# Performance work log

Hardware: AMD Instinct MI355X
Metric: run time of the kernel (lower is better)

## Reference

```python
import jax, jax.numpy as jnp
import numpy as np
import math

V = 32000      # vocab_size
CTX = 1025     # context_length (S = CTX-1)
L = 4          # num_layers
D = 1024       # hidden_dim
H = 16         # heads
DH = D // H    # head_dim
FF = 4 * D
B = 2
PAD = 3        # padding_idx / tokenizer.pad_id()


def setup_inputs() -> dict:
    key = jax.random.key(0)
    ks = jax.random.split(key, 16)
    g = lambda k, shape: jax.random.normal(k, shape, dtype=jnp.float32) * 0.02
    text = jax.random.randint(ks[0], (B, CTX), 0, V)
    emb = g(ks[1], (V, D)).at[PAD].set(0.0)   # nn.Embedding with padding_idx=3
    u = g(ks[2], (H, DH))
    v = g(ks[3], (H, DH))
    Wq = g(ks[4], (L, D, D))
    Wk = g(ks[5], (L, D, D))
    Wv = g(ks[6], (L, D, D))
    Wr = g(ks[7], (L, D, D))
    Wfc = g(ks[8], (L, D, D))
    bfc = jnp.zeros((L, D), jnp.float32)
    ln1g = jnp.ones((L, D), jnp.float32); ln1b = jnp.zeros((L, D), jnp.float32)
    ln2g = jnp.ones((L, D), jnp.float32); ln2b = jnp.zeros((L, D), jnp.float32)
    W1 = g(ks[9], (L, D, FF)); b1 = jnp.zeros((L, FF), jnp.float32)
    W2 = g(ks[10], (L, FF, D)); b2 = jnp.zeros((L, D), jnp.float32)
    lnfg = jnp.ones((D,), jnp.float32); lnfb = jnp.zeros((D,), jnp.float32)
    Wlm = g(ks[11], (D, V)); blm = jnp.zeros((V,), jnp.float32)
    return dict(text=text, emb=emb, u=u, v=v, Wq=Wq, Wk=Wk, Wv=Wv, Wr=Wr,
                Wfc=Wfc, bfc=bfc, ln1g=ln1g, ln1b=ln1b, ln2g=ln2g, ln2b=ln2b,
                W1=W1, b1=b1, W2=W2, b2=b2, lnfg=lnfg, lnfb=lnfb, Wlm=Wlm, blm=blm)


def _ln(x, g, b, eps=1e-5):
    m = x.mean(-1, keepdims=True)
    va = ((x - m) ** 2).mean(-1, keepdims=True)
    return (x - m) / jnp.sqrt(va + eps) * g + b


def _rel_shift(x):
    # Transformer-XL relative shift: pad a zero column, reshape, drop first row.
    b, h, s, r = x.shape
    xp = jnp.pad(x, ((0, 0), (0, 0), (0, 0), (1, 0)))     # (b,h,s,r+1)
    xp = xp.reshape(b, h, r + 1, s)
    return xp[:, :, 1:, :].reshape(b, h, s, r)


def _forward(text, emb, u, v, Wq, Wk, Wv, Wr, Wfc, bfc, ln1g, ln1b, ln2g, ln2b,
             W1, b1, W2, b2, lnfg, lnfb, Wlm, blm):
    ip = text[:, :-1]                 # ip_text = text[:, :-1]
    S = ip.shape[1]
    x = emb[ip]                       # (B,S,D)
    # PositionalEmbedding over Transformer-XL positions [S-1 .. 0]
    pos = jnp.arange(S - 1, -1, -1, dtype=jnp.float32)
    inv_freq = 1.0 / (10000.0 ** (jnp.arange(0, D, 2, dtype=jnp.float32) / D))
    sinu = pos[:, None] * inv_freq[None, :]
    rel = jnp.concatenate([jnp.sin(sinu), jnp.cos(sinu)], axis=-1)  # (S,D)
    # get_mask: causal triu OR pad-token rows
    causal = jnp.triu(jnp.ones((S, S), dtype=bool), 1)
    pad = (ip == PAD)
    mask = (pad[:, :, None] | causal[None]) [:, None, :, :]        # (B,1,S,S)
    full_row = mask.all(-1, keepdims=True)                          # fully-masked rows -> NaN-fill 0
    scale = 1.0 / math.sqrt(DH)
    for l in range(L):
        xn = _ln(x, ln1g[l], ln1b[l])
        q = (xn @ Wq[l]).reshape(B, S, H, DH).transpose(0, 2, 1, 3)   # (B,H,S,DH)
        k = (xn @ Wk[l]).reshape(B, S, H, DH).transpose(0, 2, 1, 3)
        vv = (xn @ Wv[l]).reshape(B, S, H, DH).transpose(0, 2, 1, 3)
        r = (rel @ Wr[l]).reshape(S, H, DH).transpose(1, 0, 2)        # (H,S,DH)
        term_AC = jnp.einsum('bhqd,bhkd->bhqk', q + u[None, :, None, :], k)
        term_BD = jnp.einsum('bhqd,hkd->bhqk', q + v[None, :, None, :], r)
        term_BD = _rel_shift(term_BD)
        scores = (term_AC + term_BD) * scale
        scores = jnp.where(mask, -1e30, scores)
        aw = jax.nn.softmax(scores, axis=-1)
        aw = jnp.where(full_row, 0.0, aw)                              # NaN -> 0 masking
        o = jnp.einsum('bhqk,bhkd->bhqd', aw, vv).transpose(0, 2, 1, 3).reshape(B, S, D)
        o = o @ Wfc[l] + bfc[l] + xn                                   # fc(out) + attn-input residual
        x = x + o                                                      # block residual
        h = _ln(x, ln2g[l], ln2b[l])
        f = jax.nn.gelu(h @ W1[l] + b1[l])
        f = jax.nn.gelu(f @ W2[l] + b2[l])
        x = x + f
    xf = _ln(x, lnfg, lnfb)
    return xf @ Wlm + blm                                              # (B,S,V) logits


def reference(text, emb, u, v, Wq, Wk, Wv, Wr, Wfc, bfc, ln1g, ln1b, ln2g, ln2b,
              W1, b1, W2, b2, lnfg, lnfb, Wlm, blm):
    return _forward(text, emb, u, v, Wq, Wk, Wv, Wr, Wfc, bfc, ln1g, ln1b,
                    ln2g, ln2b, W1, b1, W2, b2, lnfg, lnfb, Wlm, blm)
```

## Files before the change

kernel.cpp:

```cpp
#include <hip/hip_runtime.h>
#include <stdint.h>

#define S_ 1024
#define D_ 1024
#define H_ 16
#define DH_ 64
#define FF_ 4096
#define B_ 2
#define V_ 32000
#define CTX_ 1025
#define PAD_ 3

typedef unsigned short u16;
typedef __attribute__((ext_vector_type(8))) short bf16x8;
typedef __attribute__((ext_vector_type(4))) float f32x4;

enum { EPI_BF16 = 0, EPI_QKV = 1, EPI_FC = 2, EPI_GELU_BF16 = 3, EPI_GELU_RES = 4, EPI_BIAS_F32 = 5 };

__device__ __forceinline__ u16 f2bf(float f) {
  unsigned u = __float_as_uint(f);
  return (u16)((u + 0x7FFFu + ((u >> 16) & 1u)) >> 16);
}

__device__ __forceinline__ float bf2f(u16 v) {
  return __uint_as_float(((unsigned)v) << 16);
}

__device__ __forceinline__ float gelu_f(float x) {
  float t = tanhf(0.7978845608028654f * (x + 0.044715f * x * x * x));
  return 0.5f * x * (1.0f + t);
}

__device__ __forceinline__ void glds16(const void* g, void* l) {
  __builtin_amdgcn_global_load_lds(
      (const __attribute__((address_space(1))) unsigned int*)g,
      (__attribute__((address_space(3))) unsigned int*)l,
      16, 0, 0);
}

__global__ __launch_bounds__(256) void embed_gather(const int* __restrict__ text,
                                                    const float* __restrict__ emb,
                                                    float* __restrict__ x) {
  int row = blockIdx.x;
  int b = row >> 10, s = row & 1023;
  int id = text[b * CTX_ + s];
  float4 v = ((const float4*)(emb + (size_t)id * D_))[threadIdx.x];
  ((float4*)(x + (size_t)row * D_))[threadIdx.x] = v;
}

__global__ __launch_bounds__(256) void rel_enc(u16* __restrict__ rel) {
  int i = blockIdx.x;
  float pos = (float)(S_ - 1 - i);
  for (int t = threadIdx.x; t < 512; t += 256) {
    float invf = exp2f(-(float)t * (13.287712379549449f / 512.0f));
    float ang = pos * invf;
    rel[(size_t)i * D_ + t] = f2bf(sinf(ang));
    rel[(size_t)i * D_ + 512 + t] = f2bf(cosf(ang));
  }
}

__global__ __launch_bounds__(256) void wconv_t(const float* __restrict__ src,
                                               u16* __restrict__ dst, int K, int N) {
  src += (size_t)blockIdx.z * K * N;
  dst += (size_t)blockIdx.z * K * N;
  __shared__ float tile[32][33];
  int n0 = blockIdx.x * 32, k0 = blockIdx.y * 32;
  for (int idx = threadIdx.x; idx < 1024; idx += 256) {
    int r = idx >> 5, c = idx & 31;
    tile[r][c] = src[(size_t)(k0 + r) * N + n0 + c];
  }
  __syncthreads();
  for (int idx = threadIdx.x; idx < 1024; idx += 256) {
    int r = idx >> 5, c = idx & 31;
    dst[(size_t)(n0 + r) * K + k0 + c] = f2bf(tile[c][r]);
  }
}

__global__ __launch_bounds__(256) void wconv4_k(const float* __restrict__ sq,
                                                const float* __restrict__ sk,
                                                const float* __restrict__ sv,
                                                const float* __restrict__ sf,
                                                u16* __restrict__ dqkv,
                                                u16* __restrict__ dfc) {
  const int z = blockIdx.z;
  const float* src = (z == 0) ? sq : (z == 1) ? sk : (z == 2) ? sv : sf;
  u16* dst = (z < 3) ? dqkv + (size_t)z * 1024 * 1024 : dfc;
  __shared__ float tile[32][33];
  int n0 = blockIdx.x * 32, k0 = blockIdx.y * 32;
  for (int idx = threadIdx.x; idx < 1024; idx += 256) {
    int r = idx >> 5, c = idx & 31;
    tile[r][c] = src[(size_t)(k0 + r) * 1024 + n0 + c];
  }
  __syncthreads();
  for (int idx = threadIdx.x; idx < 1024; idx += 256) {
    int r = idx >> 5, c = idx & 31;
    dst[(size_t)(n0 + r) * 1024 + k0 + c] = f2bf(tile[c][r]);
  }
}

__global__ __launch_bounds__(256) void layernorm_k(const float* __restrict__ x,
                                                   const float* __restrict__ g,
                                                   const float* __restrict__ bb,
                                                   float* __restrict__ outf,
                                                   u16* __restrict__ outb) {
  int row = blockIdx.x, tid = threadIdx.x;
  const float* xr = x + (size_t)row * D_;
  float4 v = ((const float4*)xr)[tid];
  float s = v.x + v.y + v.z + v.w;
  float s2 = v.x * v.x + v.y * v.y + v.z * v.z + v.w * v.w;
  __shared__ float red[8];
#pragma unroll
  for (int off = 32; off > 0; off >>= 1) { s += __shfl_xor(s, off); s2 += __shfl_xor(s2, off); }
  if ((tid & 63) == 0) { red[tid >> 6] = s; red[4 + (tid >> 6)] = s2; }
  __syncthreads();
  s = red[0] + red[1] + red[2] + red[3];
  s2 = red[4] + red[5] + red[6] + red[7];
  float mean = s * (1.0f / D_);
  float var = s2 * (1.0f / D_) - mean * mean;
  float rstd = rsqrtf(var + 1e-5f);
  float4 gv = ((const float4*)g)[tid];
  float4 bv = ((const float4*)bb)[tid];
  float y0 = (v.x - mean) * rstd * gv.x + bv.x;
  float y1 = (v.y - mean) * rstd * gv.y + bv.y;
  float y2 = (v.z - mean) * rstd * gv.z + bv.z;
  float y3 = (v.w - mean) * rstd * gv.w + bv.w;
  if (outf) ((float4*)(outf + (size_t)row * D_))[tid] = make_float4(y0, y1, y2, y3);
  ((ushort4*)(outb + (size_t)row * D_))[tid] = make_ushort4(f2bf(y0), f2bf(y1), f2bf(y2), f2bf(y3));
}

__device__ __forceinline__ void epi_one(int mode, float v, int row, int col, int ldc,
                                        void* C0p, void* C1p, void* C2p, void* C3p,
                                        const float* bias0, const float* bias1,
                                        const float* res0) {
  if (mode == EPI_QKV) {
    int seg = col >> 10, c = col & 1023;
    size_t idx = (size_t)row * 1024 + c;
    if (seg == 0) {
      ((u16*)C0p)[idx] = f2bf(v + bias0[c]);
      ((u16*)C1p)[idx] = f2bf(v + bias1[c]);
    } else if (seg == 1) {
      ((u16*)C2p)[idx] = f2bf(v);
    } else {
      ((u16*)C3p)[idx] = f2bf(v);
    }
    return;
  }
  size_t idx = (size_t)row * ldc + col;
  float b0 = bias0 ? bias0[col] : 0.0f;
  if (mode == EPI_BF16) {
    ((u16*)C0p)[idx] = f2bf(v);
  } else if (mode == EPI_FC) {
    float* C0 = (float*)C0p;
    C0[idx] = C0[idx] + v + b0 + res0[idx];
  } else if (mode == EPI_GELU_BF16) {
    ((u16*)C0p)[idx] = f2bf(gelu_f(v + b0));
  } else if (mode == EPI_GELU_RES) {
    float* C0 = (float*)C0p;
    C0[idx] = C0[idx] + gelu_f(v + b0);
  } else {
    ((float*)C0p)[idx] = v + b0;
  }
}

__global__ __launch_bounds__(256) void gemm_bt(const u16* __restrict__ A,
                                               const u16* __restrict__ Bt,
                                               int M, int N, int K,
                                               void* __restrict__ C0p, void* __restrict__ C1p,
                                               void* __restrict__ C2p, void* __restrict__ C3p,
                                               const float* __restrict__ bias0,
                                               const float* __restrict__ bias1,
                                               const float* __restrict__ res0,
                                               int ldc, int mode) {
  __shared__ u16 lA[128 * 32];
  __shared__ u16 lB[128 * 32];
  const int tid = threadIdx.x;
  const int wave = tid >> 6, lane = tid & 63;
  unsigned gx = gridDim.x, gy = gridDim.y;
  unsigned nwg = gx * gy;
  unsigned bx = blockIdx.x, by = blockIdx.y;
  if ((nwg & 7u) == 0u) {
    unsigned lin = by * gx + bx;
    unsigned v = (lin & 7u) * (nwg >> 3) + (lin >> 3);
    bx = v / gy;
    by = v - bx * gy;
  }
  const int i0 = by * 128, j0 = bx * 128;
  const int wm = wave & 1, wn = wave >> 1;
  const int m_lane = lane & 15, quad = lane >> 4;

  f32x4 acc[4][4] = {};

  const u16* Ab = A + (size_t)i0 * K;
  const u16* Bb = Bt + (size_t)j0 * K;
  const int r0 = wave * 32 + (lane >> 2);
  const int cb = (lane & 3) * 8;

  for (int k0 = 0; k0 < K; k0 += 32) {
    glds16(Ab + (size_t)r0 * K + k0 + cb, lA + wave * 1024);
    glds16(Ab + (size_t)(r0 + 16) * K + k0 + cb, lA + wave * 1024 + 512);
    glds16(Bb + (size_t)r0 * K + k0 + cb, lB + wave * 1024);
    glds16(Bb + (size_t)(r0 + 16) * K + k0 + cb, lB + wave * 1024 + 512);
    __syncthreads();
    bf16x8 af[4], bfr[4];
#pragma unroll
    for (int t = 0; t < 4; t++) {
      af[t] = *(const bf16x8*)(lA + (wm * 64 + t * 16 + m_lane) * 32 + quad * 8);
      bfr[t] = *(const bf16x8*)(lB + (wn * 64 + t * 16 + m_lane) * 32 + quad * 8);
    }
#pragma unroll
    for (int mt = 0; mt < 4; mt++)
#pragma unroll
      for (int nt = 0; nt < 4; nt++)
        acc[mt][nt] = __builtin_amdgcn_mfma_f32_16x16x32_bf16(af[mt], bfr[nt], acc[mt][nt], 0, 0, 0);
    __syncthreads();
  }

#pragma unroll
  for (int mt = 0; mt < 4; mt++) {
#pragma unroll
    for (int nt = 0; nt < 4; nt++) {
      int col = j0 + wn * 64 + nt * 16 + m_lane;
#pragma unroll
      for (int r = 0; r < 4; r++) {
        int row = i0 + wm * 64 + mt * 16 + quad * 4 + r;
        epi_one(mode, acc[mt][nt][r], row, col, ldc, C0p, C1p, C2p, C3p, bias0, bias1, res0);
      }
    }
  }
}

__global__ __launch_bounds__(256) void gemm_bt64(const u16* __restrict__ A,
                                                 const u16* __restrict__ Bt,
                                                 int M, int N, int K,
                                                 void* __restrict__ C0p, void* __restrict__ C1p,
                                                 void* __restrict__ C2p, void* __restrict__ C3p,
                                                 const float* __restrict__ bias0,
                                                 const float* __restrict__ bias1,
                                                 const float* __restrict__ res0,
                                                 int ldc, int mode) {
  __shared__ u16 lA[64 * 32];
  __shared__ u16 lB[128 * 32];
  const int tid = threadIdx.x;
  const int wave = tid >> 6, lane = tid & 63;
  unsigned gx = gridDim.x, gy = gridDim.y;
  unsigned nwg = gx * gy;
  unsigned bx = blockIdx.x, by = blockIdx.y;
  if ((nwg & 7u) == 0u) {
    unsigned lin = by * gx + bx;
    unsigned v = (lin & 7u) * (nwg >> 3) + (lin >> 3);
    by = v / gx;
    bx = v - by * gx;
  }
  const int i0 = by * 64, j0 = bx * 128;
  const int m_lane = lane & 15, quad = lane >> 4;

  f32x4 acc[4][2] = {};

  const u16* Ab = A + (size_t)i0 * K;
  const u16* Bb = Bt + (size_t)j0 * K;
  const int rA = wave * 16 + (lane >> 2);
  const int rB = wave * 32 + (lane >> 2);
  const int cb = (lane & 3) * 8;

  for (int k0 = 0; k0 < K; k0 += 32) {
    glds16(Ab + (size_t)rA * K + k0 + cb, lA + wave * 512);
    glds16(Bb + (size_t)rB * K + k0 + cb, lB + wave * 1024);
    glds16(Bb + (size_t)(rB + 16) * K + k0 + cb, lB + wave * 1024 + 512);
    __syncthreads();
    bf16x8 af[4], bfr[2];
#pragma unroll
    for (int t = 0; t < 4; t++)
      af[t] = *(const bf16x8*)(lA + (t * 16 + m_lane) * 32 + quad * 8);
#pragma unroll
    for (int t = 0; t < 2; t++)
      bfr[t] = *(const bf16x8*)(lB + (wave * 32 + t * 16 + m_lane) * 32 + quad * 8);
#pragma unroll
    for (int mt = 0; mt < 4; mt++)
#pragma unroll
      for (int nt = 0; nt < 2; nt++)
        acc[mt][nt] = __builtin_amdgcn_mfma_f32_16x16x32_bf16(af[mt], bfr[nt], acc[mt][nt], 0, 0, 0);
    __syncthreads();
  }

#pragma unroll
  for (int mt = 0; mt < 4; mt++) {
#pragma unroll
    for (int nt = 0; nt < 2; nt++) {
      int col = j0 + wave * 32 + nt * 16 + m_lane;
#pragma unroll
      for (int r = 0; r < 4; r++) {
        int row = i0 + mt * 16 + quad * 4 + r;
        epi_one(mode, acc[mt][nt][r], row, col, ldc, C0p, C1p, C2p, C3p, bias0, bias1, res0);
      }
    }
  }
}

__global__ __launch_bounds__(256) void attn_score(const u16* __restrict__ qu,
                                                  const u16* __restrict__ qv,
                                                  const u16* __restrict__ kk,
                                                  const u16* __restrict__ rb,
                                                  float* __restrict__ scores) {
  __shared__ u16 sBD[64][132];
  const int cIdx = blockIdx.x, bh = blockIdx.y;
  int ti = (int)((sqrtf(8.0f * (float)cIdx + 1.0f) - 1.0f) * 0.5f);
  while ((ti + 1) * (ti + 2) / 2 <= cIdx) ti++;
  while (ti * (ti + 1) / 2 > cIdx) ti--;
  const int tj = cIdx - ti * (ti + 1) / 2;
  const int b = bh >> 4, h = bh & 15;
  const int tid = threadIdx.x, wave = tid >> 6, lane = tid & 63;
  const int m_lane = lane & 15, quad = lane >> 4;
  const int i0 = ti * 64, j0 = tj * 64;
  const int T0 = 15 - (ti - tj);
  const bool hasT1 = (T0 < 15);

  const u16* Qu = qu + ((size_t)(b * S_ + i0 + wave * 16 + m_lane)) * D_ + h * DH_ + quad * 8;
  const u16* Qv = qv + ((size_t)(b * S_ + i0 + wave * 16 + m_lane)) * D_ + h * DH_ + quad * 8;
  bf16x8 a0 = *(const bf16x8*)(Qu);
  bf16x8 a1 = *(const bf16x8*)(Qu + 32);
  bf16x8 c0 = *(const bf16x8*)(Qv);
  bf16x8 c1 = *(const bf16x8*)(Qv + 32);

  const u16* Kb = kk + ((size_t)(b * S_ + j0)) * D_ + h * DH_;
  const u16* R0 = rb + ((size_t)(T0 * 64)) * 4096 + h * DH_;
  const u16* R1 = R0 + (size_t)64 * 4096;

  f32x4 ac_[4] = {}, bd0_[4] = {}, bd1_[4] = {};
#pragma unroll
  for (int nt = 0; nt < 4; nt++) {
    const u16* kr = Kb + (size_t)(nt * 16 + m_lane) * D_ + quad * 8;
    bf16x8 kb0 = *(const bf16x8*)(kr);
    bf16x8 kb1 = *(const bf16x8*)(kr + 32);
    ac_[nt] = __builtin_amdgcn_mfma_f32_16x16x32_bf16(a0, kb0, ac_[nt], 0, 0, 0);
    ac_[nt] = __builtin_amdgcn_mfma_f32_16x16x32_bf16(a1, kb1, ac_[nt], 0, 0, 0);
    const u16* rr = R0 + (size_t)(nt * 16 + m_lane) * 4096 + quad * 8;
    bf16x8 rb0 = *(const bf16x8*)(rr);
    bf16x8 rb1 = *(const bf16x8*)(rr + 32);
    bd0_[nt] = __builtin_amdgcn_mfma_f32_16x16x32_bf16(c0, rb0, bd0_[nt], 0, 0, 0);
    bd0_[nt] = __builtin_amdgcn_mfma_f32_16x16x32_bf16(c1, rb1, bd0_[nt], 0, 0, 0);
    if (hasT1) {
      const u16* r2 = R1 + (size_t)(nt * 16 + m_lane) * 4096 + quad * 8;
      bf16x8 rc0 = *(const bf16x8*)(r2);
      bf16x8 rc1 = *(const bf16x8*)(r2 + 32);
      bd1_[nt] = __builtin_amdgcn_mfma_f32_16x16x32_bf16(c0, rc0, bd1_[nt], 0, 0, 0);
      bd1_[nt] = __builtin_amdgcn_mfma_f32_16x16x32_bf16(c1, rc1, bd1_[nt], 0, 0, 0);
    }
  }

#pragma unroll
  for (int nt = 0; nt < 4; nt++) {
    int col = nt * 16 + m_lane;
#pragma unroll
    for (int r = 0; r < 4; r++) {
      int row = wave * 16 + quad * 4 + r;
      sBD[row][col] = f2bf(bd0_[nt][r]);
      sBD[row][64 + col] = hasT1 ? f2bf(bd1_[nt][r]) : (u16)0;
    }
  }
  __syncthreads();

  float* C = scores + (size_t)bh * S_ * S_ + (size_t)i0 * S_ + j0;
#pragma unroll
  for (int nt = 0; nt < 4; nt++) {
    int jl = nt * 16 + m_lane;
#pragma unroll
    for (int r = 0; r < 4; r++) {
      int il = wave * 16 + quad * 4 + r;
      int tloc = jl - il + 63;
      C[(size_t)il * S_ + jl] = ac_[nt][r] + bf2f(sBD[il][tloc]);
    }
  }
}

__global__ __launch_bounds__(256) void attn_gemm(const u16* __restrict__ A, int lda,
                                                 const u16* __restrict__ Bt, int ldb,
                                                 float* __restrict__ Cf, u16* __restrict__ Cb,
                                                 int K, int mode) {
  const int ti = blockIdx.x, tj = blockIdx.y, bh = blockIdx.z;
  if (mode == 0 && tj > ti) return;
  if (mode == 1 && ti + tj < 15) return;
  const int b = bh >> 4, h = bh & 15;
  __shared__ u16 lA[64 * 64];
  __shared__ u16 lB[64 * 64];
  const int tid = threadIdx.x, wave = tid >> 6, lane = tid & 63;
  const int m_lane = lane & 15, quad = lane >> 4;
  const int i0 = ti * 64, j0 = tj * 64;

  size_t aoff, boff;
  if (mode == 0)      { aoff = (size_t)b * S_ * D_ + h * DH_; boff = (size_t)b * S_ * D_ + h * DH_; }
  else if (mode == 1) { aoff = (size_t)b * S_ * D_ + h * DH_; boff = (size_t)h * DH_; }
  else                { aoff = (size_t)bh * S_ * S_;          boff = (size_t)bh * DH_ * S_; }
  const u16* Ap = A + aoff + (size_t)i0 * lda;
  const u16* Bp = Bt + boff + (mode == 2 ? (size_t)0 : (size_t)j0 * ldb);

  f32x4 acc[4] = {};
  const int cid0 = wave * 128 + lane, cid1 = cid0 + 64;
  const int ar0 = cid0 >> 3, ac0 = (cid0 & 7) * 8;
  const int ar1 = cid1 >> 3, ac1 = (cid1 & 7) * 8;

  const int Kend = (mode == 2) ? (ti + 1) * 64 : K;
  for (int k0 = 0; k0 < Kend; k0 += 64) {
    glds16(Ap + (size_t)ar0 * lda + k0 + ac0, lA + wave * 1024);
    glds16(Ap + (size_t)ar1 * lda + k0 + ac1, lA + wave * 1024 + 512);
    glds16(Bp + (size_t)ar0 * ldb + k0 + ac0, lB + wave * 1024);
    glds16(Bp + (size_t)ar1 * ldb + k0 + ac1, lB + wave * 1024 + 512);
    __syncthreads();
    bf16x8 a0 = *(const bf16x8*)(lA + (wave * 16 + m_lane) * 64 + quad * 8);
    bf16x8 a1 = *(const bf16x8*)(lA + (wave * 16 + m_lane) * 64 + 32 + quad * 8);
#pragma unroll
    for (int nt = 0; nt < 4; nt++) {
      bf16x8 b0 = *(const bf16x8*)(lB + (nt * 16 + m_lane) * 64 + quad * 8);
      bf16x8 b1 = *(const bf16x8*)(lB + (nt * 16 + m_lane) * 64 + 32 + quad * 8);
      acc[nt] = __builtin_amdgcn_mfma_f32_16x16x32_bf16(a0, b0, acc[nt], 0, 0, 0);
      acc[nt] = __builtin_amdgcn_mfma_f32_16x16x32_bf16(a1, b1, acc[nt], 0, 0, 0);
    }
    __syncthreads();
  }

  if (mode == 0) {
    float* C = Cf + (size_t)bh * S_ * S_;
#pragma unroll
    for (int nt = 0; nt < 4; nt++) {
      int col = j0 + nt * 16 + m_lane;
#pragma unroll
      for (int r = 0; r < 4; r++) {
        int row = i0 + wave * 16 + quad * 4 + r;
        C[(size_t)row * S_ + col] = acc[nt][r];
      }
    }
  } else if (mode == 1) {
    float* C = Cf + (size_t)bh * S_ * S_;
#pragma unroll
    for (int nt = 0; nt < 4; nt++) {
      int t = j0 + nt * 16 + m_lane;
#pragma unroll
      for (int r = 0; r < 4; r++) {
        int row = i0 + wave * 16 + quad * 4 + r;
        int j = row + t - (S_ - 1);
        if (j >= 0) C[(size_t)row * S_ + j] += acc[nt][r];
      }
    }
  } else {
    u16* C = Cb + (size_t)b * S_ * D_ + h * DH_;
#pragma unroll
    for (int nt = 0; nt < 4; nt++) {
      int col = nt * 16 + m_lane;
#pragma unroll
      for (int r = 0; r < 4; r++) {
        int row = i0 + wave * 16 + quad * 4 + r;
        C[(size_t)row * D_ + col] = f2bf(acc[nt][r]);
      }
    }
  }
}

__global__ __launch_bounds__(256) void softmax_k(const float* __restrict__ scores,
                                                 u16* __restrict__ aw,
                                                 const int* __restrict__ text) {
  const int i = blockIdx.x, bh = blockIdx.y, b = bh >> 4;
  const float* s = scores + ((size_t)bh * S_ + i) * S_;
  u16* o = aw + ((size_t)bh * S_ + i) * S_;
  const int tid = threadIdx.x, wave = tid >> 6, lane = tid & 63;
  const int n = i + 1;
  const int jmax = ((i >> 6) + 1) << 6;
  const int j0 = tid * 4;
  if (text[b * CTX_ + i] == PAD_) {
    if (j0 < jmax) ((ushort4*)o)[tid] = make_ushort4(0, 0, 0, 0);
    return;
  }
  const float scale = 0.125f;
  float4 sv = make_float4(0.f, 0.f, 0.f, 0.f);
  if (j0 < jmax) sv = ((const float4*)s)[tid];
  float e0 = (j0 + 0 < n) ? sv.x * scale : -3e38f;
  float e1 = (j0 + 1 < n) ? sv.y * scale : -3e38f;
  float e2 = (j0 + 2 < n) ? sv.z * scale : -3e38f;
  float e3 = (j0 + 3 < n) ? sv.w * scale : -3e38f;
  float mx = fmaxf(fmaxf(e0, e1), fmaxf(e2, e3));
  __shared__ float red[8];
#pragma unroll
  for (int off = 32; off > 0; off >>= 1) mx = fmaxf(mx, __shfl_xor(mx, off));
  if (lane == 0) red[wave] = mx;
  __syncthreads();
  mx = fmaxf(fmaxf(red[0], red[1]), fmaxf(red[2], red[3]));
  float p0 = __expf(e0 - mx);
  float p1 = __expf(e1 - mx);
  float p2 = __expf(e2 - mx);
  float p3 = __expf(e3 - mx);
  float sum = p0 + p1 + p2 + p3;
#pragma unroll
  for (int off = 32; off > 0; off >>= 1) sum += __shfl_xor(sum, off);
  if (lane == 0) red[4 + wave] = sum;
  __syncthreads();
  sum = red[4] + red[5] + red[6] + red[7];
  float inv = 1.0f / sum;
  if (j0 < jmax)
    ((ushort4*)o)[tid] = make_ushort4(f2bf(p0 * inv), f2bf(p1 * inv), f2bf(p2 * inv), f2bf(p3 * inv));
}

__global__ __launch_bounds__(256) void v_transpose(const u16* __restrict__ v,
                                                   u16* __restrict__ vT) {
  int bh = blockIdx.y, b = bh >> 4, h = bh & 15;
  int j0 = blockIdx.x * 64;
  __shared__ u16 tile[64][65];
  for (int idx = threadIdx.x; idx < 4096; idx += 256) {
    int jj = idx >> 6, d = idx & 63;
    tile[jj][d] = v[(size_t)(b * S_ + j0 + jj) * D_ + h * DH_ + d];
  }
  __syncthreads();
  for (int idx = threadIdx.x; idx < 4096; idx += 256) {
    int d = idx >> 6, jj = idx & 63;
    vT[((size_t)bh * DH_ + d) * S_ + j0 + jj] = tile[jj][d];
  }
}

extern "C" void kernel_launch(void* const* d_in, const int* in_sizes, int n_in,
                              void* d_out, int out_size, void* d_ws, size_t ws_size,
                              hipStream_t stream) {
  (void)in_sizes; (void)n_in; (void)out_size;
  const int* text = (const int*)d_in[0];
  const float* emb = (const float*)d_in[1];
  const float* u_in = (const float*)d_in[2];
  const float* v_in = (const float*)d_in[3];
  const float* Wq = (const float*)d_in[4];
  const float* Wk = (const float*)d_in[5];
  const float* Wv = (const float*)d_in[6];
  const float* Wr = (const float*)d_in[7];
  const float* Wfc = (const float*)d_in[8];
  const float* bfc = (const float*)d_in[9];
  const float* ln1g = (const float*)d_in[10];
  const float* ln1b = (const float*)d_in[11];
  const float* ln2g = (const float*)d_in[12];
  const float* ln2b = (const float*)d_in[13];
  const float* W1 = (const float*)d_in[14];
  const float* b1 = (const float*)d_in[15];
  const float* W2 = (const float*)d_in[16];
  const float* b2 = (const float*)d_in[17];
  const float* lnfg = (const float*)d_in[18];
  const float* lnfb = (const float*)d_in[19];
  const float* Wlm = (const float*)d_in[20];
  const float* blm = (const float*)d_in[21];
  float* out = (float*)d_out;

  char* w = (char*)d_ws;
  size_t off = 0;
  auto alloc = [&](size_t bytes) -> void* {
    void* p = w + off;
    off += (bytes + 255) & ~(size_t)255;
    return p;
  };
  float* x      = (float*)alloc(2048ull * 1024 * 4);
  float* xnf    = (float*)alloc(2048ull * 1024 * 4);
  u16* xnb      = (u16*)alloc(2048ull * 1024 * 2);
  u16* relb     = (u16*)alloc(1024ull * 1024 * 2);
  u16* wqkvt    = (u16*)alloc(3072ull * 1024 * 2);
  u16* wrt_all  = (u16*)alloc(4096ull * 1024 * 2);
  u16* wfct     = (u16*)alloc(1024ull * 1024 * 2);
  u16* w1t      = (u16*)alloc(4096ull * 1024 * 2);
  u16* w2t      = (u16*)alloc(4096ull * 1024 * 2);
  u16* wlmt     = (u16*)alloc(32000ull * 1024 * 2);
  u16* qu       = (u16*)alloc(2048ull * 1024 * 2);
  u16* qv       = (u16*)alloc(2048ull * 1024 * 2);
  u16* kk       = (u16*)alloc(2048ull * 1024 * 2);
  u16* vv       = (u16*)alloc(2048ull * 1024 * 2);
  u16* vT       = (u16*)alloc(2048ull * 1024 * 2);
  u16* rb_all   = (u16*)alloc(1024ull * 4096 * 2);
  float* scores = (float*)alloc(32ull * 1024 * 1024 * 4);
  u16* aw       = (u16*)alloc(32ull * 1024 * 1024 * 2);
  u16* o_       = (u16*)alloc(2048ull * 1024 * 2);
  u16* f1       = (u16*)alloc(2048ull * 4096 * 2);
  if (off > ws_size) return;

  dim3 blk(256);
  embed_gather<<<2048, blk, 0, stream>>>(text, emb, x);
  rel_enc<<<1024, blk, 0, stream>>>(relb);
  wconv_t<<<dim3(1000, 32), blk, 0, stream>>>(Wlm, wlmt, 1024, 32000);
  wconv_t<<<dim3(32, 32, 4), blk, 0, stream>>>(Wr, wrt_all, 1024, 1024);
  gemm_bt<<<dim3(32, 8), blk, 0, stream>>>(relb, wrt_all, 1024, 4096, 1024,
                                           rb_all, nullptr, nullptr, nullptr,
                                           nullptr, nullptr, nullptr, 4096, EPI_BF16);

  for (int l = 0; l < 4; l++) {
    const size_t dd = 1048576;
    wconv4_k<<<dim3(32, 32, 4), blk, 0, stream>>>(Wq + l * dd, Wk + l * dd, Wv + l * dd,
                                                  Wfc + l * dd, wqkvt, wfct);
    wconv_t<<<dim3(128, 32), blk, 0, stream>>>(W1 + l * 4ull * dd, w1t, 1024, 4096);
    wconv_t<<<dim3(32, 128), blk, 0, stream>>>(W2 + l * 4ull * dd, w2t, 4096, 1024);

    layernorm_k<<<2048, blk, 0, stream>>>(x, ln1g + l * 1024, ln1b + l * 1024, xnf, xnb);

    gemm_bt<<<dim3(24, 16), blk, 0, stream>>>(xnb, wqkvt, 2048, 3072, 1024,
                                              qu, qv, kk, vv, u_in, v_in, nullptr, 1024, EPI_QKV);
    v_transpose<<<dim3(16, 32), blk, 0, stream>>>(vv, vT);

    attn_score<<<dim3(136, 32), blk, 0, stream>>>(qu, qv, kk, rb_all + (size_t)l * 1024, scores);
    softmax_k<<<dim3(1024, 32), blk, 0, stream>>>(scores, aw, text);
    attn_gemm<<<dim3(16, 1, 32), blk, 0, stream>>>(aw, 1024, vT, 1024, nullptr, o_, 1024, 2);

    gemm_bt64<<<dim3(8, 32), blk, 0, stream>>>(o_, wfct, 2048, 1024, 1024,
                                               x, nullptr, nullptr, nullptr,
                                               bfc + l * 1024, nullptr, xnf, 1024, EPI_FC);
    layernorm_k<<<2048, blk, 0, stream>>>(x, ln2g + l * 1024, ln2b + l * 1024, nullptr, xnb);
    gemm_bt<<<dim3(32, 16), blk, 0, stream>>>(xnb, w1t, 2048, 4096, 1024,
                                              f1, nullptr, nullptr, nullptr,
                                              b1 + l * 4096, nullptr, nullptr, 4096, EPI_GELU_BF16);
    gemm_bt64<<<dim3(8, 32), blk, 0, stream>>>(f1, w2t, 2048, 1024, 4096,
                                               x, nullptr, nullptr, nullptr,
                                               b2 + l * 1024, nullptr, nullptr, 1024, EPI_GELU_RES);
  }

  layernorm_k<<<2048, blk, 0, stream>>>(x, lnfg, lnfb, nullptr, xnb);
  gemm_bt<<<dim3(250, 16), blk, 0, stream>>>(xnb, wlmt, 2048, 32000, 1024,
                                             out, nullptr, nullptr, nullptr,
                                             blm, nullptr, nullptr, 32000, EPI_BIAS_F32);
}
```

Before: 2.349 ms.

## Double GEMM K-tile to 64 and XOR-swizzle LDS layout to avoid bank conflicts

The two dense GEMM kernels now stage 64-wide K slices per iteration instead of 32, which halves the number of barriers and loop iterations and doubles the MFMA work between syncs. All three GEMM kernels, including the attention one, write LDS rows with an XOR swizzle on the 16-byte chunk index and read fragments back with the matching swizzle. This is meant to remove LDS bank conflicts on the fragment reads. The cost is double the shared memory per block in the dense GEMMs, which may lower occupancy.

Result: no change. 2.311 ms (-1.6%).

```diff
diff --git a/kernel.cpp b/kernel.cpp
--- a/kernel.cpp
+++ b/kernel.cpp
@@ -171,8 +171,8 @@
                                                const float* __restrict__ bias1,
                                                const float* __restrict__ res0,
                                                int ldc, int mode) {
-  __shared__ u16 lA[128 * 32];
-  __shared__ u16 lB[128 * 32];
+  __shared__ u16 lA[128 * 64];
+  __shared__ u16 lB[128 * 64];
   const int tid = threadIdx.x;
   const int wave = tid >> 6, lane = tid & 63;
   unsigned gx = gridDim.x, gy = gridDim.y;
@@ -192,20 +192,36 @@
 
   const u16* Ab = A + (size_t)i0 * K;
   const u16* Bb = Bt + (size_t)j0 * K;
-  const int r0 = wave * 32 + (lane >> 2);
-  const int cb = (lane & 3) * 8;
-
-  for (int k0 = 0; k0 < K; k0 += 32) {
-    glds16(Ab + (size_t)r0 * K + k0 + cb, lA + wave * 1024);
-    glds16(Ab + (size_t)(r0 + 16) * K + k0 + cb, lA + wave * 1024 + 512);
-    glds16(Bb + (size_t)r0 * K + k0 + cb, lB + wave * 1024);
-    glds16(Bb + (size_t)(r0 + 16) * K + k0 + cb, lB + wave * 1024 + 512);
+  const int sr = lane >> 3;
+  const int sc = ((lane & 7) ^ sr) * 8;
+
+  for (int k0 = 0; k0 < K; k0 += 64) {
+#pragma unroll
+    for (int c = 0; c < 4; c++) {
+      int row = wave * 32 + c * 8 + sr;
+      glds16(Ab + (size_t)row * K + k0 + sc, lA + (size_t)(wave * 32 + c * 8) * 64);
+      glds16(Bb + (size_t)row * K + k0 + sc, lB + (size_t)(wave * 32 + c * 8) * 64);
+    }
     __syncthreads();
     bf16x8 af[4], bfr[4];
 #pragma unroll
     for (int t = 0; t < 4; t++) {
-      af[t] = *(const bf16x8*)(lA + (wm * 64 + t * 16 + m_lane) * 32 + quad * 8);
-      bfr[t] = *(const bf16x8*)(lB + (wn * 64 + t * 16 + m_lane) * 32 + quad * 8);
+      int ra = wm * 64 + t * 16 + m_lane;
+      int rb_ = wn * 64 + t * 16 + m_lane;
+      af[t]  = *(const bf16x8*)(lA + ra * 64 + ((quad ^ (ra & 7)) * 8));
+      bfr[t] = *(const bf16x8*)(lB + rb_ * 64 + ((quad ^ (rb_ & 7)) * 8));
+    }
+#pragma unroll
+    for (int mt = 0; mt < 4; mt++)
+#pragma unroll
+      for (int nt = 0; nt < 4; nt++)
+        acc[mt][nt] = __builtin_amdgcn_mfma_f32_16x16x32_bf16(af[mt], bfr[nt], acc[mt][nt], 0, 0, 0);
+#pragma unroll
+    for (int t = 0; t < 4; t++) {
+      int ra = wm * 64 + t * 16 + m_lane;
+      int rb_ = wn * 64 + t * 16 + m_lane;
+      af[t]  = *(const bf16x8*)(lA + ra * 64 + (((4 + quad) ^ (ra & 7)) * 8));
+      bfr[t] = *(const bf16x8*)(lB + rb_ * 64 + (((4 + quad) ^ (rb_ & 7)) * 8));
     }
 #pragma unroll
     for (int mt = 0; mt < 4; mt++)
@@ -238,8 +254,8 @@
                                                  const float* __restrict__ bias1,
                                                  const float* __restrict__ res0,
                                                  int ldc, int mode) {
-  __shared__ u16 lA[64 * 32];
-  __shared__ u16 lB[128 * 32];
+  __shared__ u16 lA[64 * 64];
+  __shared__ u16 lB[128 * 64];
   const int tid = threadIdx.x;
   const int wave = tid >> 6, lane = tid & 63;
   unsigned gx = gridDim.x, gy = gridDim.y;
@@ -258,22 +274,47 @@
 
   const u16* Ab = A + (size_t)i0 * K;
   const u16* Bb = Bt + (size_t)j0 * K;
-  const int rA = wave * 16 + (lane >> 2);
-  const int rB = wave * 32 + (lane >> 2);
-  const int cb = (lane & 3) * 8;
-
-  for (int k0 = 0; k0 < K; k0 += 32) {
-    glds16(Ab + (size_t)rA * K + k0 + cb, lA + wave * 512);
-    glds16(Bb + (size_t)rB * K + k0 + cb, lB + wave * 1024);
-    glds16(Bb + (size_t)(rB + 16) * K + k0 + cb, lB + wave * 1024 + 512);
+  const int sr = lane >> 3;
+  const int sc = ((lane & 7) ^ sr) * 8;
+
+  for (int k0 = 0; k0 < K; k0 += 64) {
+#pragma unroll
+    for (int c = 0; c < 2; c++) {
+      int row = wave * 16 + c * 8 + sr;
+      glds16(Ab + (size_t)row * K + k0 + sc, lA + (size_t)(wave * 16 + c * 8) * 64);
+    }
+#pragma unroll
+    for (int c = 0; c < 4; c++) {
+      int row = wave * 32 + c * 8 + sr;
+      glds16(Bb + (size_t)row * K + k0 + sc, lB + (size_t)(wave * 32 + c * 8) * 64);
+    }
     __syncthreads();
     bf16x8 af[4], bfr[2];
 #pragma unroll
-    for (int t = 0; t < 4; t++)
-      af[t] = *(const bf16x8*)(lA + (t * 16 + m_lane) * 32 + quad * 8);
-#pragma unroll
-    for (int t = 0; t < 2; t++)
-      bfr[t] = *(const bf16x8*)(lB + (wave * 32 + t * 16 + m_lane) * 32 + quad * 8);
+    for (int t = 0; t < 4; t++) {
+      int ra = t * 16 + m_lane;
+      af[t] = *(const bf16x8*)(lA + ra * 64 + ((quad ^ (ra & 7)) * 8));
+    }
+#pragma unroll
+    for (int t = 0; t < 2; t++) {
+      int rb_ = wave * 32 + t * 16 + m_lane;
+      bfr[t] = *(const bf16x8*)(lB + rb_ * 64 + ((quad ^ (rb_ & 7)) * 8));
+    }
+#pragma unroll
+    for (int mt = 0; mt < 4; mt++)
+#pragma unroll
+      for (int nt = 0; nt < 2; nt++)
+        acc[mt][nt] = __builtin_amdgcn_mfma_f32_16x16x32_bf16(af[mt], bfr[nt], acc[mt][nt], 0, 0, 0);
+#pragma unroll
+    for (int t = 0; t < 4; t++) {
+      int ra = t * 16 + m_lane;
+      af[t] = *(const bf16x8*)(lA + ra * 64 + (((4 + quad) ^ (ra & 7)) * 8));
+    }
+#pragma unroll
+    for (int t = 0; t < 2; t++) {
+      int rb_ = wave * 32 + t * 16 + m_lane;
+      bfr[t] = *(const bf16x8*)(lB + rb_ * 64 + (((4 + quad) ^ (rb_ & 7)) * 8));
+    }
 #pragma unroll
     for (int mt = 0; mt < 4; mt++)
 #pragma unroll
@@ -394,23 +435,26 @@
   const u16* Bp = Bt + boff + (mode == 2 ? (size_t)0 : (size_t)j0 * ldb);
 
   f32x4 acc[4] = {};
-  const int cid0 = wave * 128 + lane, cid1 = cid0 + 64;
-  const int ar0 = cid0 >> 3, ac0 = (cid0 & 7) * 8;
-  const int ar1 = cid1 >> 3, ac1 = (cid1 & 7) * 8;
+  const int sr = lane >> 3;
+  const int sc = ((lane & 7) ^ sr) * 8;
 
   const int Kend = (mode == 2) ? (ti + 1) * 64 : K;
   for (int k0 = 0; k0 < Kend; k0 += 64) {
-    glds16(Ap + (size_t)ar0 * lda + k0 + ac0, lA + wave * 1024);
-    glds16(Ap + (size_t)ar1 * lda + k0 + ac1, lA + wave * 1024 + 512);
-    glds16(Bp + (size_t)ar0 * ldb + k0 + ac0, lB + wave * 1024);
-    glds16(Bp + (size_t)ar1 * ldb + k0 + ac1, lB + wave * 1024 + 512);
+#pragma unroll
+    for (int c = 0; c < 2; c++) {
+      int row = wave * 16 + c * 8 + sr;
+      glds16(Ap + (size_t)row * lda + k0 + sc, lA + (size_t)(wave * 16 + c * 8) * 64);
+      glds16(Bp + (size_t)row * ldb + k0 + sc, lB + (size_t)(wave * 16 + c * 8) * 64);
+    }
     __syncthreads();
-    bf16x8 a0 = *(const bf16x8*)(lA + (wave * 16 + m_lane) * 64 + quad * 8);
-    bf16x8 a1 = *(const bf16x8*)(lA + (wave * 16 + m_lane) * 64 + 32 + quad * 8);
+    int ra = wave * 16 + m_lane;
+    bf16x8 a0 = *(const bf16x8*)(lA + ra * 64 + ((quad ^ (ra & 7)) * 8));
+    bf16x8 a1 = *(const bf16x8*)(lA + ra * 64 + (((4 + quad) ^ (ra & 7)) * 8));
 #pragma unroll
     for (int nt = 0; nt < 4; nt++) {
-      bf16x8 b0 = *(const bf16x8*)(lB + (nt * 16 + m_lane) * 64 + quad * 8);
-      bf16x8 b1 = *(const bf16x8*)(lB + (nt * 16 + m_lane) * 64 + 32 + quad * 8);
+      int rb_ = nt * 16 + m_lane;
+      bf16x8 b0 = *(const bf16x8*)(lB + rb_ * 64 + ((quad ^ (rb_ & 7)) * 8));
+      bf16x8 b1 = *(const bf16x8*)(lB + rb_ * 64 + (((4 + quad) ^ (rb_ & 7)) * 8));
       acc[nt] = __builtin_amdgcn_mfma_f32_16x16x32_bf16(a0, b0, acc[nt], 0, 0, 0);
       acc[nt] = __builtin_amdgcn_mfma_f32_16x16x32_bf16(a1, b1, acc[nt], 0, 0, 0);
     }
```
